# Performance work log

Measured on AMD Instinct MI355X. Metric: run time of the kernel, lower is better.

The kernel has to match this reference:

```python
import jax, jax.numpy as jnp
import numpy as np


def setup_inputs() -> dict:
    key = jax.random.key(0)
    k1, k2 = jax.random.split(key)
    B, T, D, K = 8, 4096, 256, 1024
    z = jax.random.normal(k1, (B, T, D), dtype=jnp.float32)
    codebook = jax.random.uniform(k2, (K, D), dtype=jnp.float32)
    return {"z": z, "codebook": codebook}


def reference(z, codebook):
    # Squared L2 distance via dot-product decomposition (same argmin as
    # the broadcasted squared-difference in the original module, without
    # materializing the (B,T,K,D) intermediate).
    #   ||z - c||^2 = ||z||^2 - 2 z.c + ||c||^2
    z_sq = jnp.sum(z * z, axis=-1, keepdims=True)            # (B,T,1)
    c_sq = jnp.sum(codebook * codebook, axis=-1)             # (K,)
    cross = jnp.einsum("btd,kd->btk", z, codebook)           # (B,T,K)
    l2_distance = z_sq - 2.0 * cross + c_sq                  # (B,T,K)
    codebook_indices = jnp.argmin(l2_distance, axis=-1)      # (B,T)
    z_q = codebook[codebook_indices]                         # (B,T,D)
    # Straight-through estimator
    z_q = z + jax.lax.stop_gradient(z_q - z)
    return (z_q, codebook_indices)
```

## Files before the change

### kernel.cpp

```cpp
#include <hip/hip_runtime.h>
#include <math.h>

#define NTOK   32768
#define NDIM   256
#define NCODE  1024
#define NSTRIP 8
#define CHUNK  (128 * 32)

typedef _Float16 f16x8 __attribute__((ext_vector_type(8)));
typedef float    f32x4 __attribute__((ext_vector_type(4)));

__device__ __forceinline__ void gld_lds16(const void* g, void* l) {
    __builtin_amdgcn_global_load_lds(
        (const __attribute__((address_space(1))) void*)g,
        (__attribute__((address_space(3))) void*)l, 16, 0, 0);
}

__global__ __launch_bounds__(256) void prep_cb(
        const float* __restrict__ cb,
        _Float16* __restrict__ ch, _Float16* __restrict__ cl,
        float* __restrict__ csq) {
    const int L   = blockIdx.x * 256 + threadIdx.x;
    const int row = L >> 5;
    const int g   = L & 31;

    const float* src = cb + (size_t)row * NDIM + g * 8;
    float4 a0 = *(const float4*)src;
    float4 a1 = *(const float4*)(src + 4);
    float v[8] = {a0.x, a0.y, a0.z, a0.w, a1.x, a1.y, a1.z, a1.w};
    f16x8 hi, lo;
    float s = 0.f;
    #pragma unroll
    for (int e = 0; e < 8; ++e) {
        _Float16 h = (_Float16)v[e];
        hi[e] = h;
        lo[e] = (_Float16)(v[e] - (float)h);
        s += v[e] * v[e];
    }
    const size_t dst = (size_t)((row >> 7) * 8 + (g >> 2)) * CHUNK
                     + (row & 127) * 32 + (g & 3) * 8;
    *(f16x8*)&ch[dst] = hi;
    *(f16x8*)&cl[dst] = lo;
    #pragma unroll
    for (int off = 16; off > 0; off >>= 1) s += __shfl_down(s, off, 32);
    if ((threadIdx.x & 31) == 0) csq[row] = s;
}

__global__ __launch_bounds__(256, 2) void vq_main(
        const float* __restrict__ z,
        const _Float16* __restrict__ ch, const _Float16* __restrict__ cl,
        const float* __restrict__ csq, const float* __restrict__ cb,
        float* __restrict__ zq, float* __restrict__ io) {
    __shared__ _Float16 Bh[4 * CHUNK];
    __shared__ _Float16 Bl[4 * CHUNK];

    const int tid  = threadIdx.x;
    const int w    = tid >> 6;
    const int lane = tid & 63;
    const int quad = lane >> 4, lr = lane & 15;
    const int my   = w >> 1, nx = w & 1;
    const int m0   = blockIdx.x * 64;

    f16x8 ah[2][8], al[2][8];
    #pragma unroll
    for (int mt = 0; mt < 2; ++mt) {
        const float* zp = z + (size_t)(m0 + my * 32 + mt * 16 + lr) * NDIM
                        + quad * 8;
        #pragma unroll
        for (int c = 0; c < 8; ++c) {
            float4 a0 = *(const float4*)(zp + c * 32);
            float4 a1 = *(const float4*)(zp + c * 32 + 4);
            float v[8] = {a0.x, a0.y, a0.z, a0.w, a1.x, a1.y, a1.z, a1.w};
            #pragma unroll
            for (int e = 0; e < 8; ++e) {
                _Float16 h = (_Float16)v[e];
                ah[mt][c][e] = h;
                al[mt][c][e] = (_Float16)(v[e] - (float)h);
            }
        }
    }

    float bv[2][4];
    int   bi[2][4];
    #pragma unroll
    for (int mt = 0; mt < 2; ++mt)
        #pragma unroll
        for (int r = 0; r < 4; ++r) { bv[mt][r] = INFINITY; bi[mt][r] = 0x7fffffff; }

    f32x4 acc[2][4];
    #pragma unroll
    for (int mt = 0; mt < 2; ++mt)
        #pragma unroll
        for (int t = 0; t < 4; ++t) acc[mt][t] = (f32x4){0.f, 0.f, 0.f, 0.f};

    for (int strip = 0; strip < NSTRIP; ++strip) {
        float cs[4];
        #pragma unroll
        for (int t = 0; t < 4; ++t)
            cs[t] = csq[strip * 128 + (nx * 4 + t) * 16 + lr];

        #pragma unroll
        for (int kh = 0; kh < 2; ++kh) {
            __syncthreads();
            {
                const size_t base = (size_t)(strip * 8 + kh * 4 + w) * CHUNK
                                  + lane * 8;
                const _Float16* sh = ch + base;
                const _Float16* sl = cl + base;
                #pragma unroll
                for (int i = 0; i < 8; ++i) {
                    gld_lds16(sh + i * 512, Bh + w * CHUNK + i * 512);
                    gld_lds16(sl + i * 512, Bl + w * CHUNK + i * 512);
                }
            }
            __syncthreads();

            #pragma unroll
            for (int k4 = 0; k4 < 4; ++k4) {
                const int kg = kh * 4 + k4;
                f16x8 fbh[4], fbl[4];
                #pragma unroll
                for (int t = 0; t < 4; ++t) {
                    const int off = k4 * CHUNK
                                  + ((nx * 4 + t) * 16 + lr) * 32 + quad * 8;
                    fbh[t] = *(const f16x8*)&Bh[off];
                    fbl[t] = *(const f16x8*)&Bl[off];
                }
                #pragma unroll
                for (int mt = 0; mt < 2; ++mt)
                    #pragma unroll
                    for (int t = 0; t < 4; ++t) {
                        acc[mt][t] = __builtin_amdgcn_mfma_f32_16x16x32_f16(
                                         ah[mt][kg], fbh[t], acc[mt][t], 0, 0, 0);
                        acc[mt][t] = __builtin_amdgcn_mfma_f32_16x16x32_f16(
                                         al[mt][kg], fbh[t], acc[mt][t], 0, 0, 0);
                        acc[mt][t] = __builtin_amdgcn_mfma_f32_16x16x32_f16(
                                         ah[mt][kg], fbl[t], acc[mt][t], 0, 0, 0);
                    }
            }
        }

        #pragma unroll
        for (int mt = 0; mt < 2; ++mt)
            #pragma unroll
            for (int r = 0; r < 4; ++r)
                #pragma unroll
                for (int t = 0; t < 4; ++t) {
                    float v = cs[t] - 2.0f * acc[mt][t][r];
                    int   n = strip * 128 + (nx * 4 + t) * 16 + lr;
                    if (v < bv[mt][r] || (v == bv[mt][r] && n < bi[mt][r])) {
                        bv[mt][r] = v; bi[mt][r] = n;
                    }
                }
        #pragma unroll
        for (int mt = 0; mt < 2; ++mt)
            #pragma unroll
            for (int t = 0; t < 4; ++t) acc[mt][t] = (f32x4){0.f, 0.f, 0.f, 0.f};
    }

    #pragma unroll
    for (int msk = 1; msk < 16; msk <<= 1)
        #pragma unroll
        for (int mt = 0; mt < 2; ++mt)
            #pragma unroll
            for (int r = 0; r < 4; ++r) {
                float ov = __shfl_xor(bv[mt][r], msk, 64);
                int   oi = __shfl_xor(bi[mt][r], msk, 64);
                if (ov < bv[mt][r] || (ov == bv[mt][r] && oi < bi[mt][r])) {
                    bv[mt][r] = ov; bi[mt][r] = oi;
                }
            }

    __syncthreads();
    float* sval  = (float*)Bh;
    int*   sidx  = (int*)&Bh[512];
    int*   bestS = (int*)&Bh[1024];

    if (lr == 0) {
        #pragma unroll
        for (int mt = 0; mt < 2; ++mt)
            #pragma unroll
            for (int r = 0; r < 4; ++r) {
                int row = my * 32 + mt * 16 + quad * 4 + r;
                sval[row * 2 + nx] = bv[mt][r];
                sidx[row * 2 + nx] = bi[mt][r];
            }
    }
    __syncthreads();

    if (tid < 64) {
        float v0 = sval[tid * 2], v1 = sval[tid * 2 + 1];
        int   i0 = sidx[tid * 2], i1 = sidx[tid * 2 + 1];
        bool take1 = (v1 < v0) || (v1 == v0 && i1 < i0);
        int best = take1 ? i1 : i0;
        bestS[tid] = best;
        io[m0 + tid] = (float)best;
    }
    __syncthreads();

    const int tr = tid >> 4, tc = tid & 15;
    #pragma unroll
    for (int p = 0; p < 4; ++p) {
        int row = p * 16 + tr;
        const float* src = cb + (size_t)bestS[row] * NDIM;
        float*       dst = zq + (size_t)(m0 + row) * NDIM;
        #pragma unroll
        for (int q = 0; q < 4; ++q) {
            int col = q * 64 + tc * 4;
            *(float4*)&dst[col] = *(const float4*)&src[col];
        }
    }
}

extern "C" void kernel_launch(void* const* d_in, const int* in_sizes, int n_in,
                              void* d_out, int out_size, void* d_ws, size_t ws_size,
                              hipStream_t stream) {
    const float* z  = (const float*)d_in[0];
    const float* cb = (const float*)d_in[1];

    float* zq = (float*)d_out;
    float* io = (float*)d_out + (size_t)NTOK * NDIM;

    _Float16* ch  = (_Float16*)d_ws;
    _Float16* cl  = ch + (size_t)NCODE * NDIM;
    float*    csq = (float*)(cl + (size_t)NCODE * NDIM);

    prep_cb<<<NCODE * 32 / 256, 256, 0, stream>>>(cb, ch, cl, csq);

    vq_main<<<NTOK / 64, 256, 0, stream>>>(z, ch, cl, csq, cb, zq, io);
}
```

Measured before the change: 132.6 us.

## Double-buffer codebook LDS tiles with 512-thread blocks and conflict-free layout

Blocks grow to 512 threads covering 128 tokens, so each codebook tile staged in LDS is reused by twice as many rows. The codebook hi/lo tiles are now double-buffered: the next half-strip is issued with global_load_lds while the current one is consumed, using explicit vmcnt waits and raw barriers in place of a full sync pair. The packed codebook layout is rearranged so each lane's 16-byte LDS reads are contiguous, which is meant to cut bank conflicts, and MFMA bursts raise wave priority with s_setprio. LDS use doubles to 128 KB per block, which with launch_bounds(512,2) may limit occupancy, and the hand-set vmcnt counts depend on the exact number of loads issued.

```diff
diff --git a/kernel.cpp b/kernel.cpp
--- a/kernel.cpp
+++ b/kernel.cpp
@@ -4,8 +4,7 @@
 #define NTOK   32768
 #define NDIM   256
 #define NCODE  1024
-#define NSTRIP 8
-#define CHUNK  (128 * 32)
+#define CHUNK  4096
 
 typedef _Float16 f16x8 __attribute__((ext_vector_type(8)));
 typedef float    f32x4 __attribute__((ext_vector_type(4)));
@@ -37,8 +36,9 @@
         lo[e] = (_Float16)(v[e] - (float)h);
         s += v[e] * v[e];
     }
+    const int r = row & 127;
     const size_t dst = (size_t)((row >> 7) * 8 + (g >> 2)) * CHUNK
-                     + (row & 127) * 32 + (g & 3) * 8;
+                     + (r >> 4) * 512 + (g & 3) * 128 + (r & 15) * 8;
     *(f16x8*)&ch[dst] = hi;
     *(f16x8*)&cl[dst] = lo;
     #pragma unroll
@@ -46,20 +46,60 @@
     if ((threadIdx.x & 31) == 0) csq[row] = s;
 }
 
-__global__ __launch_bounds__(256, 2) void vq_main(
+
+#define STAGE(h, buf)                                                          \
+    do {                                                                       \
+        const size_t _sb = (size_t)(h) * 16384 + (size_t)tid * 8;              \
+        _Pragma("unroll")                                                      \
+        for (int _i = 0; _i < 4; ++_i) {                                       \
+            gld_lds16(ch + _sb + _i * 4096, &Bs[buf][0][w * 512 + _i * 4096]); \
+            gld_lds16(cl + _sb + _i * 4096, &Bs[buf][1][w * 512 + _i * 4096]); \
+        }                                                                      \
+    } while (0)
+
+#define COMPUTE(kh, buf)                                                       \
+    do {                                                                       \
+        _Pragma("unroll")                                                      \
+        for (int _k4 = 0; _k4 < 4; ++_k4) {                                    \
+            f16x8 fbh[4], fbl[4];                                              \
+            _Pragma("unroll")                                                  \
+            for (int _t = 0; _t < 4; ++_t) {                                   \
+                const int _off = _k4 * 4096 + (nx * 4 + _t) * 512              \
+                               + quad * 128 + lr * 8;                          \
+                fbh[_t] = *(const f16x8*)&Bs[buf][0][_off];                    \
+                fbl[_t] = *(const f16x8*)&Bs[buf][1][_off];                    \
+            }                                                                  \
+            __builtin_amdgcn_s_setprio(1);                                     \
+            _Pragma("unroll")                                                  \
+            for (int _mt = 0; _mt < 2; ++_mt)                                  \
+                _Pragma("unroll")                                              \
+                for (int _t = 0; _t < 4; ++_t) {                               \
+                    acc[_mt][_t] = __builtin_amdgcn_mfma_f32_16x16x32_f16(     \
+                        ah[_mt][(kh) * 4 + _k4], fbh[_t], acc[_mt][_t], 0, 0, 0); \
+                    acc[_mt][_t] = __builtin_amdgcn_mfma_f32_16x16x32_f16(     \
+                        al[_mt][(kh) * 4 + _k4], fbh[_t], acc[_mt][_t], 0, 0, 0); \
+                    acc[_mt][_t] = __builtin_amdgcn_mfma_f32_16x16x32_f16(     \
+                        ah[_mt][(kh) * 4 + _k4], fbl[_t], acc[_mt][_t], 0, 0, 0); \
+                }                                                              \
+            __builtin_amdgcn_s_setprio(0);                                     \
+        }                                                                      \
+    } while (0)
+
+__global__ __launch_bounds__(512, 2) void vq_main(
         const float* __restrict__ z,
         const _Float16* __restrict__ ch, const _Float16* __restrict__ cl,
         const float* __restrict__ csq, const float* __restrict__ cb,
         float* __restrict__ zq, float* __restrict__ io) {
-    __shared__ _Float16 Bh[4 * CHUNK];
-    __shared__ _Float16 Bl[4 * CHUNK];
+    __shared__ _Float16 Bs[2][2][16384];
 
     const int tid  = threadIdx.x;
     const int w    = tid >> 6;
     const int lane = tid & 63;
     const int quad = lane >> 4, lr = lane & 15;
     const int my   = w >> 1, nx = w & 1;
-    const int m0   = blockIdx.x * 64;
+    const int m0   = blockIdx.x * 128;
+
+    STAGE(0, 0);
 
     f16x8 ah[2][8], al[2][8];
     #pragma unroll
@@ -93,52 +133,31 @@
         #pragma unroll
         for (int t = 0; t < 4; ++t) acc[mt][t] = (f32x4){0.f, 0.f, 0.f, 0.f};
 
-    for (int strip = 0; strip < NSTRIP; ++strip) {
+    for (int strip = 0; strip < 8; ++strip) {
         float cs[4];
         #pragma unroll
         for (int t = 0; t < 4; ++t)
             cs[t] = csq[strip * 128 + (nx * 4 + t) * 16 + lr];
 
-        #pragma unroll
-        for (int kh = 0; kh < 2; ++kh) {
-            __syncthreads();
-            {
-                const size_t base = (size_t)(strip * 8 + kh * 4 + w) * CHUNK
-                                  + lane * 8;
-                const _Float16* sh = ch + base;
-                const _Float16* sl = cl + base;
-                #pragma unroll
-                for (int i = 0; i < 8; ++i) {
-                    gld_lds16(sh + i * 512, Bh + w * CHUNK + i * 512);
-                    gld_lds16(sl + i * 512, Bl + w * CHUNK + i * 512);
-                }
-            }
-            __syncthreads();
-
-            #pragma unroll
-            for (int k4 = 0; k4 < 4; ++k4) {
-                const int kg = kh * 4 + k4;
-                f16x8 fbh[4], fbl[4];
-                #pragma unroll
-                for (int t = 0; t < 4; ++t) {
-                    const int off = k4 * CHUNK
-                                  + ((nx * 4 + t) * 16 + lr) * 32 + quad * 8;
-                    fbh[t] = *(const f16x8*)&Bh[off];
-                    fbl[t] = *(const f16x8*)&Bl[off];
-                }
-                #pragma unroll
-                for (int mt = 0; mt < 2; ++mt)
-                    #pragma unroll
-                    for (int t = 0; t < 4; ++t) {
-                        acc[mt][t] = __builtin_amdgcn_mfma_f32_16x16x32_f16(
-                                         ah[mt][kg], fbh[t], acc[mt][t], 0, 0, 0);
-                        acc[mt][t] = __builtin_amdgcn_mfma_f32_16x16x32_f16(
-                                         al[mt][kg], fbh[t], acc[mt][t], 0, 0, 0);
-                        acc[mt][t] = __builtin_amdgcn_mfma_f32_16x16x32_f16(
-                                         ah[mt][kg], fbl[t], acc[mt][t], 0, 0, 0);
-                    }
-            }
+        STAGE(2 * strip + 1, 1);
+        asm volatile("s_waitcnt vmcnt(12)" ::: "memory");
+        __builtin_amdgcn_s_barrier();
+        __builtin_amdgcn_sched_barrier(0);
+        COMPUTE(0, 0);
+        __builtin_amdgcn_sched_barrier(0);
+        __builtin_amdgcn_s_barrier();
+
+        if (strip < 7) {
+            STAGE(2 * strip + 2, 0);
+            asm volatile("s_waitcnt vmcnt(8)" ::: "memory");
+        } else {
+            asm volatile("s_waitcnt vmcnt(0)" ::: "memory");
         }
+        __builtin_amdgcn_s_barrier();
+        __builtin_amdgcn_sched_barrier(0);
+        COMPUTE(1, 1);
+        __builtin_amdgcn_sched_barrier(0);
+        __builtin_amdgcn_s_barrier();
 
         #pragma unroll
         for (int mt = 0; mt < 2; ++mt)
@@ -172,9 +191,9 @@
             }
 
     __syncthreads();
-    float* sval  = (float*)Bh;
-    int*   sidx  = (int*)&Bh[512];
-    int*   bestS = (int*)&Bh[1024];
+    float* sval  = (float*)&Bs[0][0][0];
+    int*   sidx  = (int*)(sval + 256);
+    int*   bestS = (int*)(sval + 512);
 
     if (lr == 0) {
         #pragma unroll
@@ -188,7 +207,7 @@
     }
     __syncthreads();
 
-    if (tid < 64) {
+    if (tid < 128) {
         float v0 = sval[tid * 2], v1 = sval[tid * 2 + 1];
         int   i0 = sidx[tid * 2], i1 = sidx[tid * 2 + 1];
         bool take1 = (v1 < v0) || (v1 == v0 && i1 < i0);
@@ -201,7 +220,7 @@
     const int tr = tid >> 4, tc = tid & 15;
     #pragma unroll
     for (int p = 0; p < 4; ++p) {
-        int row = p * 16 + tr;
+        int row = p * 32 + tr;
         const float* src = cb + (size_t)bestS[row] * NDIM;
         float*       dst = zq + (size_t)(m0 + row) * NDIM;
         #pragma unroll
@@ -227,5 +246,5 @@
 
     prep_cb<<<NCODE * 32 / 256, 256, 0, stream>>>(cb, ch, cl, csq);
 
-    vq_main<<<NTOK / 64, 256, 0, stream>>>(z, ch, cl, csq, cb, zq, io);
-}
+    vq_main<<<NTOK / 128, 512, 0, stream>>>(z, ch, cl, csq, cb, zq, io);
+}
```

Result: slower. 151.6 us (+14.3%).

## Pipeline codebook chunks through a 4-slot LDS ring with async prefetch

Applied to the files above, without the earlier changes.

Replaces the load-all-then-compute scheme (two syncthreads per 4-chunk batch) with a 4-deep ring buffer of per-k chunks. Each phase prefetches chunk p+3 with global_load_lds while computing on chunk p, using vmcnt waits and raw barriers. The codebook layout is reshuffled so each lane reads its fragment more contiguously, csq is staged in LDS, and MFMA blocks run at raised priority. The aim is to hide global-load latency behind MFMA work, at the cost of more barriers and tighter hand-managed wait counts.

```diff
diff --git a/kernel.cpp b/kernel.cpp
--- a/kernel.cpp
+++ b/kernel.cpp
@@ -4,8 +4,7 @@
 #define NTOK   32768
 #define NDIM   256
 #define NCODE  1024
-#define NSTRIP 8
-#define CHUNK  (128 * 32)
+#define CHUNK  4096
 
 typedef _Float16 f16x8 __attribute__((ext_vector_type(8)));
 typedef float    f32x4 __attribute__((ext_vector_type(4)));
@@ -37,22 +36,81 @@
         lo[e] = (_Float16)(v[e] - (float)h);
         s += v[e] * v[e];
     }
+    const int r = row & 127;
     const size_t dst = (size_t)((row >> 7) * 8 + (g >> 2)) * CHUNK
-                     + (row & 127) * 32 + (g & 3) * 8;
+                     + (r >> 4) * 512 + (g & 3) * 128 + (r & 15) * 8;
     *(f16x8*)&ch[dst] = hi;
     *(f16x8*)&cl[dst] = lo;
     #pragma unroll
     for (int off = 16; off > 0; off >>= 1) s += __shfl_down(s, off, 32);
     if ((threadIdx.x & 31) == 0) csq[row] = s;
 }
+
+
+#define PHASE(p, GB, DOSTAGE, WK, FIRSTZ) do {                               \
+    const int _sl = (p) & 3;                                                 \
+    f16x8 fbh[4], fbl[4];                                                    \
+    _Pragma("unroll")                                                        \
+    for (int _t = 0; _t < 4; ++_t) {                                         \
+        fbh[_t] = *(const f16x8*)&Bs[_sl][0][boff[_t]];                      \
+        fbl[_t] = *(const f16x8*)&Bs[_sl][1][boff[_t]];                      \
+    }                                                                        \
+    if (DOSTAGE) {                                                           \
+        const size_t _s  = (size_t)((GB) + (p) + 3) * CHUNK + tid * 8;       \
+        const int    _dsl = ((p) + 3) & 3;                                   \
+        const int    _d   = tid * 8;                                         \
+        gld_lds16(ch + _s,        &Bs[_dsl][0][_d]);                         \
+        gld_lds16(ch + _s + 2048, &Bs[_dsl][0][_d + 2048]);                  \
+        gld_lds16(cl + _s,        &Bs[_dsl][1][_d]);                         \
+        gld_lds16(cl + _s + 2048, &Bs[_dsl][1][_d + 2048]);                  \
+    }                                                                        \
+    asm volatile("s_waitcnt vmcnt(" #WK ")" ::: "memory");                   \
+    __builtin_amdgcn_s_barrier();                                            \
+    asm volatile("s_waitcnt lgkmcnt(0)" ::: "memory");                       \
+    __builtin_amdgcn_s_setprio(1);                                           \
+    _Pragma("unroll")                                                        \
+    for (int _mt = 0; _mt < 2; ++_mt)                                        \
+        _Pragma("unroll")                                                    \
+        for (int _t = 0; _t < 4; ++_t) {                                     \
+            acc[_mt][_t] = __builtin_amdgcn_mfma_f32_16x16x32_f16(           \
+                ah[_mt][(p)], fbh[_t],                                       \
+                (FIRSTZ) ? zz : acc[_mt][_t], 0, 0, 0);                      \
+            acc[_mt][_t] = __builtin_amdgcn_mfma_f32_16x16x32_f16(           \
+                al[_mt][(p)], fbh[_t], acc[_mt][_t], 0, 0, 0);               \
+            acc[_mt][_t] = __builtin_amdgcn_mfma_f32_16x16x32_f16(           \
+                ah[_mt][(p)], fbl[_t], acc[_mt][_t], 0, 0, 0);               \
+        }                                                                    \
+    __builtin_amdgcn_s_setprio(0);                                           \
+    __builtin_amdgcn_s_barrier();                                            \
+} while (0)
+
+#define FOLD(S) do {                                                         \
+    float cs[4];                                                             \
+    _Pragma("unroll")                                                        \
+    for (int _t = 0; _t < 4; ++_t)                                           \
+        cs[_t] = csq_lds[(S) * 128 + (nx * 4 + _t) * 16 + lr];               \
+    _Pragma("unroll")                                                        \
+    for (int _mt = 0; _mt < 2; ++_mt)                                        \
+        _Pragma("unroll")                                                    \
+        for (int _r = 0; _r < 4; ++_r)                                       \
+            _Pragma("unroll")                                                \
+            for (int _t = 0; _t < 4; ++_t) {                                 \
+                float _v = cs[_t] - 2.0f * acc[_mt][_t][_r];                 \
+                int   _n = (S) * 128 + (nx * 4 + _t) * 16 + lr;              \
+                if (_v < bv[_mt][_r] ||                                      \
+                    (_v == bv[_mt][_r] && _n < bi[_mt][_r])) {               \
+                    bv[_mt][_r] = _v; bi[_mt][_r] = _n;                      \
+                }                                                            \
+            }                                                                \
+} while (0)
 
 __global__ __launch_bounds__(256, 2) void vq_main(
         const float* __restrict__ z,
         const _Float16* __restrict__ ch, const _Float16* __restrict__ cl,
         const float* __restrict__ csq, const float* __restrict__ cb,
         float* __restrict__ zq, float* __restrict__ io) {
-    __shared__ _Float16 Bh[4 * CHUNK];
-    __shared__ _Float16 Bl[4 * CHUNK];
+    __shared__ _Float16 Bs[4][2][4096];
+    __shared__ float    csq_lds[1024];
 
     const int tid  = threadIdx.x;
     const int w    = tid >> 6;
@@ -60,6 +118,16 @@
     const int quad = lane >> 4, lr = lane & 15;
     const int my   = w >> 1, nx = w & 1;
     const int m0   = blockIdx.x * 64;
+
+    gld_lds16(csq + tid * 4, &csq_lds[tid * 4]);
+    #pragma unroll
+    for (int c = 0; c < 3; ++c) {
+        const size_t sb = (size_t)c * CHUNK + tid * 8;
+        gld_lds16(ch + sb,        &Bs[c][0][tid * 8]);
+        gld_lds16(ch + sb + 2048, &Bs[c][0][tid * 8 + 2048]);
+        gld_lds16(cl + sb,        &Bs[c][1][tid * 8]);
+        gld_lds16(cl + sb + 2048, &Bs[c][1][tid * 8 + 2048]);
+    }
 
     f16x8 ah[2][8], al[2][8];
     #pragma unroll
@@ -80,6 +148,11 @@
         }
     }
 
+    int boff[4];
+    #pragma unroll
+    for (int t = 0; t < 4; ++t)
+        boff[t] = (nx * 4 + t) * 512 + quad * 128 + lr * 8;
+
     float bv[2][4];
     int   bi[2][4];
     #pragma unroll
@@ -87,75 +160,39 @@
         #pragma unroll
         for (int r = 0; r < 4; ++r) { bv[mt][r] = INFINITY; bi[mt][r] = 0x7fffffff; }
 
+    const f32x4 zz = (f32x4){0.f, 0.f, 0.f, 0.f};
     f32x4 acc[2][4];
     #pragma unroll
     for (int mt = 0; mt < 2; ++mt)
         #pragma unroll
-        for (int t = 0; t < 4; ++t) acc[mt][t] = (f32x4){0.f, 0.f, 0.f, 0.f};
-
-    for (int strip = 0; strip < NSTRIP; ++strip) {
-        float cs[4];
-        #pragma unroll
-        for (int t = 0; t < 4; ++t)
-            cs[t] = csq[strip * 128 + (nx * 4 + t) * 16 + lr];
-
-        #pragma unroll
-        for (int kh = 0; kh < 2; ++kh) {
-            __syncthreads();
-            {
-                const size_t base = (size_t)(strip * 8 + kh * 4 + w) * CHUNK
-                                  + lane * 8;
-                const _Float16* sh = ch + base;
-                const _Float16* sl = cl + base;
-                #pragma unroll
-                for (int i = 0; i < 8; ++i) {
-                    gld_lds16(sh + i * 512, Bh + w * CHUNK + i * 512);
-                    gld_lds16(sl + i * 512, Bl + w * CHUNK + i * 512);
-                }
-            }
-            __syncthreads();
-
-            #pragma unroll
-            for (int k4 = 0; k4 < 4; ++k4) {
-                const int kg = kh * 4 + k4;
-                f16x8 fbh[4], fbl[4];
-                #pragma unroll
-                for (int t = 0; t < 4; ++t) {
-                    const int off = k4 * CHUNK
-                                  + ((nx * 4 + t) * 16 + lr) * 32 + quad * 8;
-                    fbh[t] = *(const f16x8*)&Bh[off];
-                    fbl[t] = *(const f16x8*)&Bl[off];
-                }
-                #pragma unroll
-                for (int mt = 0; mt < 2; ++mt)
-                    #pragma unroll
-                    for (int t = 0; t < 4; ++t) {
-                        acc[mt][t] = __builtin_amdgcn_mfma_f32_16x16x32_f16(
-                                         ah[mt][kg], fbh[t], acc[mt][t], 0, 0, 0);
-                        acc[mt][t] = __builtin_amdgcn_mfma_f32_16x16x32_f16(
-                                         al[mt][kg], fbh[t], acc[mt][t], 0, 0, 0);
-                        acc[mt][t] = __builtin_amdgcn_mfma_f32_16x16x32_f16(
-                                         ah[mt][kg], fbl[t], acc[mt][t], 0, 0, 0);
-                    }
-            }
-        }
-
-        #pragma unroll
-        for (int mt = 0; mt < 2; ++mt)
-            #pragma unroll
-            for (int r = 0; r < 4; ++r)
-                #pragma unroll
-                for (int t = 0; t < 4; ++t) {
-                    float v = cs[t] - 2.0f * acc[mt][t][r];
-                    int   n = strip * 128 + (nx * 4 + t) * 16 + lr;
-                    if (v < bv[mt][r] || (v == bv[mt][r] && n < bi[mt][r])) {
-                        bv[mt][r] = v; bi[mt][r] = n;
-                    }
-                }
-        #pragma unroll
-        for (int mt = 0; mt < 2; ++mt)
-            #pragma unroll
-            for (int t = 0; t < 4; ++t) acc[mt][t] = (f32x4){0.f, 0.f, 0.f, 0.f};
+        for (int t = 0; t < 4; ++t) acc[mt][t] = zz;
+
+    asm volatile("s_waitcnt vmcnt(0)" ::: "memory");
+    __syncthreads();
+
+    for (int s = 0; s < 7; ++s) {
+        const int gb = s * 8;
+        PHASE(0, gb, 1, 8, 1);
+        PHASE(1, gb, 1, 8, 0);
+        PHASE(2, gb, 1, 8, 0);
+        PHASE(3, gb, 1, 8, 0);
+        PHASE(4, gb, 1, 8, 0);
+        PHASE(5, gb, 1, 8, 0);
+        PHASE(6, gb, 1, 8, 0);
+        PHASE(7, gb, 1, 8, 0);
+        FOLD(s);
+    }
+    {
+        const int gb = 56;
+        PHASE(0, gb, 1, 8, 1);
+        PHASE(1, gb, 1, 8, 0);
+        PHASE(2, gb, 1, 8, 0);
+        PHASE(3, gb, 1, 8, 0);
+        PHASE(4, gb, 1, 8, 0);
+        PHASE(5, gb, 0, 4, 0);
+        PHASE(6, gb, 0, 0, 0);
+        PHASE(7, gb, 0, 0, 0);
+        FOLD(7);
     }
 
     #pragma unroll
@@ -172,9 +209,9 @@
             }
 
     __syncthreads();
-    float* sval  = (float*)Bh;
-    int*   sidx  = (int*)&Bh[512];
-    int*   bestS = (int*)&Bh[1024];
+    float* sval  = (float*)&Bs[0][0][0];
+    int*   sidx  = (int*)&Bs[0][0][512];
+    int*   bestS = (int*)&Bs[0][0][1024];
 
     if (lr == 0) {
         #pragma unroll
```

Measured after the change: 133.9 us. No clear change (+0.9%).

## Split-K across 16 waves with direct global fragment loads and LDS partial reduction

Applied to the files above, without the earlier changes.

Grows the block to 1024 threads and splits the 256-wide reduction dimension across two wave groups. Each wave loads codebook fragments straight from global memory in a pre-swizzled MFMA layout instead of staging them through LDS, and partial sums are combined through a double-buffered LDS exchange. It also raises MFMA issue priority around the compute. The aim is more waves to hide latency and the removal of the LDS staging traffic. In exchange it adds a barrier per strip, redundant global and L2 reads of the codebook, and a larger register footprint per thread under launch_bounds 1024.

```diff
diff --git a/kernel.cpp b/kernel.cpp
--- a/kernel.cpp
+++ b/kernel.cpp
@@ -4,17 +4,10 @@
 #define NTOK   32768
 #define NDIM   256
 #define NCODE  1024
-#define NSTRIP 8
-#define CHUNK  (128 * 32)
+#define CHUNK  4096
 
 typedef _Float16 f16x8 __attribute__((ext_vector_type(8)));
 typedef float    f32x4 __attribute__((ext_vector_type(4)));
-
-__device__ __forceinline__ void gld_lds16(const void* g, void* l) {
-    __builtin_amdgcn_global_load_lds(
-        (const __attribute__((address_space(1))) void*)g,
-        (__attribute__((address_space(3))) void*)l, 16, 0, 0);
-}
 
 __global__ __launch_bounds__(256) void prep_cb(
         const float* __restrict__ cb,
@@ -37,8 +30,9 @@
         lo[e] = (_Float16)(v[e] - (float)h);
         s += v[e] * v[e];
     }
+    const int r = row & 127;
     const size_t dst = (size_t)((row >> 7) * 8 + (g >> 2)) * CHUNK
-                     + (row & 127) * 32 + (g & 3) * 8;
+                     + (r >> 4) * 512 + (g & 3) * 128 + (r & 15) * 8;
     *(f16x8*)&ch[dst] = hi;
     *(f16x8*)&cl[dst] = lo;
     #pragma unroll
@@ -46,28 +40,30 @@
     if ((threadIdx.x & 31) == 0) csq[row] = s;
 }
 
-__global__ __launch_bounds__(256, 2) void vq_main(
+__global__ __launch_bounds__(1024) void vq_main(
         const float* __restrict__ z,
         const _Float16* __restrict__ ch, const _Float16* __restrict__ cl,
         const float* __restrict__ csq, const float* __restrict__ cb,
         float* __restrict__ zq, float* __restrict__ io) {
-    __shared__ _Float16 Bh[4 * CHUNK];
-    __shared__ _Float16 Bl[4 * CHUNK];
+    __shared__ float mbuf[2][8][64][16];
 
     const int tid  = threadIdx.x;
     const int w    = tid >> 6;
     const int lane = tid & 63;
     const int quad = lane >> 4, lr = lane & 15;
-    const int my   = w >> 1, nx = w & 1;
+    const int kh   = w >> 3;
+    const int my   = (w >> 2) & 1;
+    const int nx   = w & 3;
+    const int w4   = (my << 2) | nx;
     const int m0   = blockIdx.x * 64;
 
-    f16x8 ah[2][8], al[2][8];
+    f16x8 ah[2][4], al[2][4];
     #pragma unroll
     for (int mt = 0; mt < 2; ++mt) {
         const float* zp = z + (size_t)(m0 + my * 32 + mt * 16 + lr) * NDIM
-                        + quad * 8;
-        #pragma unroll
-        for (int c = 0; c < 8; ++c) {
+                        + kh * 128 + quad * 8;
+        #pragma unroll
+        for (int c = 0; c < 4; ++c) {
             float4 a0 = *(const float4*)(zp + c * 32);
             float4 a1 = *(const float4*)(zp + c * 32 + 4);
             float v[8] = {a0.x, a0.y, a0.z, a0.w, a1.x, a1.y, a1.z, a1.w};
@@ -80,6 +76,9 @@
         }
     }
 
+    const int boff0 = (nx * 2) * 512 + quad * 128 + lr * 8;
+    const int boff1 = boff0 + 512;
+
     float bv[2][4];
     int   bi[2][4];
     #pragma unroll
@@ -87,128 +86,128 @@
         #pragma unroll
         for (int r = 0; r < 4; ++r) { bv[mt][r] = INFINITY; bi[mt][r] = 0x7fffffff; }
 
-    f32x4 acc[2][4];
-    #pragma unroll
-    for (int mt = 0; mt < 2; ++mt)
-        #pragma unroll
-        for (int t = 0; t < 4; ++t) acc[mt][t] = (f32x4){0.f, 0.f, 0.f, 0.f};
-
-    for (int strip = 0; strip < NSTRIP; ++strip) {
-        float cs[4];
-        #pragma unroll
-        for (int t = 0; t < 4; ++t)
-            cs[t] = csq[strip * 128 + (nx * 4 + t) * 16 + lr];
-
-        #pragma unroll
-        for (int kh = 0; kh < 2; ++kh) {
-            __syncthreads();
-            {
-                const size_t base = (size_t)(strip * 8 + kh * 4 + w) * CHUNK
-                                  + lane * 8;
-                const _Float16* sh = ch + base;
-                const _Float16* sl = cl + base;
+    const f32x4 zz = (f32x4){0.f, 0.f, 0.f, 0.f};
+    f32x4 acc[2][2];
+
+    for (int s = 0; s < 8; ++s) {
+        const size_t cbase = (size_t)(s * 8 + kh * 4) * CHUNK;
+        #pragma unroll
+        for (int c = 0; c < 4; ++c) {
+            const _Float16* ph = ch + cbase + (size_t)c * CHUNK;
+            const _Float16* pl = cl + cbase + (size_t)c * CHUNK;
+            f16x8 bh0 = *(const f16x8*)&ph[boff0];
+            f16x8 bh1 = *(const f16x8*)&ph[boff1];
+            f16x8 bl0 = *(const f16x8*)&pl[boff0];
+            f16x8 bl1 = *(const f16x8*)&pl[boff1];
+            __builtin_amdgcn_s_setprio(1);
+            #pragma unroll
+            for (int mt = 0; mt < 2; ++mt) {
+                acc[mt][0] = __builtin_amdgcn_mfma_f32_16x16x32_f16(
+                    ah[mt][c], bh0, (c == 0) ? zz : acc[mt][0], 0, 0, 0);
+                acc[mt][0] = __builtin_amdgcn_mfma_f32_16x16x32_f16(
+                    al[mt][c], bh0, acc[mt][0], 0, 0, 0);
+                acc[mt][0] = __builtin_amdgcn_mfma_f32_16x16x32_f16(
+                    ah[mt][c], bl0, acc[mt][0], 0, 0, 0);
+                acc[mt][1] = __builtin_amdgcn_mfma_f32_16x16x32_f16(
+                    ah[mt][c], bh1, (c == 0) ? zz : acc[mt][1], 0, 0, 0);
+                acc[mt][1] = __builtin_amdgcn_mfma_f32_16x16x32_f16(
+                    al[mt][c], bh1, acc[mt][1], 0, 0, 0);
+                acc[mt][1] = __builtin_amdgcn_mfma_f32_16x16x32_f16(
+                    ah[mt][c], bl1, acc[mt][1], 0, 0, 0);
+            }
+            __builtin_amdgcn_s_setprio(0);
+        }
+
+        const int par = s & 1;
+        if (kh) {
+            float* mp = &mbuf[par][w4][lane][0];
+            *(f32x4*)(mp +  0) = acc[0][0];
+            *(f32x4*)(mp +  4) = acc[0][1];
+            *(f32x4*)(mp +  8) = acc[1][0];
+            *(f32x4*)(mp + 12) = acc[1][1];
+        }
+        __syncthreads();
+        if (!kh) {
+            float cs0 = csq[s * 128 + (nx * 2) * 16 + lr];
+            float cs1 = csq[s * 128 + (nx * 2 + 1) * 16 + lr];
+            const float* mp = &mbuf[par][w4][lane][0];
+            f32x4 p00 = *(const f32x4*)(mp +  0);
+            f32x4 p01 = *(const f32x4*)(mp +  4);
+            f32x4 p10 = *(const f32x4*)(mp +  8);
+            f32x4 p11 = *(const f32x4*)(mp + 12);
+            #pragma unroll
+            for (int mt = 0; mt < 2; ++mt) {
+                f32x4 d0 = (mt == 0) ? p00 : p10;
+                f32x4 d1 = (mt == 0) ? p01 : p11;
                 #pragma unroll
-                for (int i = 0; i < 8; ++i) {
-                    gld_lds16(sh + i * 512, Bh + w * CHUNK + i * 512);
-                    gld_lds16(sl + i * 512, Bl + w * CHUNK + i * 512);
-                }
-            }
-            __syncthreads();
-
-            #pragma unroll
-            for (int k4 = 0; k4 < 4; ++k4) {
-                const int kg = kh * 4 + k4;
-                f16x8 fbh[4], fbl[4];
-                #pragma unroll
-                for (int t = 0; t < 4; ++t) {
-                    const int off = k4 * CHUNK
-                                  + ((nx * 4 + t) * 16 + lr) * 32 + quad * 8;
-                    fbh[t] = *(const f16x8*)&Bh[off];
-                    fbl[t] = *(const f16x8*)&Bl[off];
-                }
-                #pragma unroll
-                for (int mt = 0; mt < 2; ++mt)
-                    #pragma unroll
-                    for (int t = 0; t < 4; ++t) {
-                        acc[mt][t] = __builtin_amdgcn_mfma_f32_16x16x32_f16(
-                                         ah[mt][kg], fbh[t], acc[mt][t], 0, 0, 0);
-                        acc[mt][t] = __builtin_amdgcn_mfma_f32_16x16x32_f16(
-                                         al[mt][kg], fbh[t], acc[mt][t], 0, 0, 0);
-                        acc[mt][t] = __builtin_amdgcn_mfma_f32_16x16x32_f16(
-                                         ah[mt][kg], fbl[t], acc[mt][t], 0, 0, 0);
+                for (int r = 0; r < 4; ++r) {
+                    float v0 = cs0 - 2.0f * (acc[mt][0][r] + d0[r]);
+                    int   n0 = s * 128 + (nx * 2) * 16 + lr;
+                    if (v0 < bv[mt][r] || (v0 == bv[mt][r] && n0 < bi[mt][r])) {
+                        bv[mt][r] = v0; bi[mt][r] = n0;
                     }
-            }
-        }
-
-        #pragma unroll
-        for (int mt = 0; mt < 2; ++mt)
-            #pragma unroll
-            for (int r = 0; r < 4; ++r)
-                #pragma unroll
-                for (int t = 0; t < 4; ++t) {
-                    float v = cs[t] - 2.0f * acc[mt][t][r];
-                    int   n = strip * 128 + (nx * 4 + t) * 16 + lr;
-                    if (v < bv[mt][r] || (v == bv[mt][r] && n < bi[mt][r])) {
-                        bv[mt][r] = v; bi[mt][r] = n;
+                    float v1 = cs1 - 2.0f * (acc[mt][1][r] + d1[r]);
+                    int   n1 = s * 128 + (nx * 2 + 1) * 16 + lr;
+                    if (v1 < bv[mt][r] || (v1 == bv[mt][r] && n1 < bi[mt][r])) {
+                        bv[mt][r] = v1; bi[mt][r] = n1;
                     }
                 }
-        #pragma unroll
-        for (int mt = 0; mt < 2; ++mt)
-            #pragma unroll
-            for (int t = 0; t < 4; ++t) acc[mt][t] = (f32x4){0.f, 0.f, 0.f, 0.f};
-    }
-
-    #pragma unroll
-    for (int msk = 1; msk < 16; msk <<= 1)
-        #pragma unroll
-        for (int mt = 0; mt < 2; ++mt)
-            #pragma unroll
-            for (int r = 0; r < 4; ++r) {
-                float ov = __shfl_xor(bv[mt][r], msk, 64);
-                int   oi = __shfl_xor(bi[mt][r], msk, 64);
-                if (ov < bv[mt][r] || (ov == bv[mt][r] && oi < bi[mt][r])) {
-                    bv[mt][r] = ov; bi[mt][r] = oi;
+            }
+        }
+    }
+
+    if (!kh) {
+        #pragma unroll
+        for (int msk = 1; msk < 16; msk <<= 1)
+            #pragma unroll
+            for (int mt = 0; mt < 2; ++mt)
+                #pragma unroll
+                for (int r = 0; r < 4; ++r) {
+                    float ov = __shfl_xor(bv[mt][r], msk, 64);
+                    int   oi = __shfl_xor(bi[mt][r], msk, 64);
+                    if (ov < bv[mt][r] || (ov == bv[mt][r] && oi < bi[mt][r])) {
+                        bv[mt][r] = ov; bi[mt][r] = oi;
+                    }
                 }
-            }
-
-    __syncthreads();
-    float* sval  = (float*)Bh;
-    int*   sidx  = (int*)&Bh[512];
-    int*   bestS = (int*)&Bh[1024];
-
-    if (lr == 0) {
+    }
+
+    float* sval  = &mbuf[0][0][0][0];
+    int*   sidx  = (int*)(sval + 256);
+    int*   bestS = (int*)(sval + 512);
+
+    if (!kh && lr == 0) {
         #pragma unroll
         for (int mt = 0; mt < 2; ++mt)
             #pragma unroll
             for (int r = 0; r < 4; ++r) {
                 int row = my * 32 + mt * 16 + quad * 4 + r;
-                sval[row * 2 + nx] = bv[mt][r];
-                sidx[row * 2 + nx] = bi[mt][r];
+                sval[row * 4 + nx] = bv[mt][r];
+                sidx[row * 4 + nx] = bi[mt][r];
             }
     }
     __syncthreads();
 
     if (tid < 64) {
-        float v0 = sval[tid * 2], v1 = sval[tid * 2 + 1];
-        int   i0 = sidx[tid * 2], i1 = sidx[tid * 2 + 1];
-        bool take1 = (v1 < v0) || (v1 == v0 && i1 < i0);
-        int best = take1 ? i1 : i0;
-        bestS[tid] = best;
-        io[m0 + tid] = (float)best;
+        float bvv = sval[tid * 4];
+        int   bii = sidx[tid * 4];
+        #pragma unroll
+        for (int k = 1; k < 4; ++k) {
+            float v = sval[tid * 4 + k];
+            int   i = sidx[tid * 4 + k];
+            if (v < bvv || (v == bvv && i < bii)) { bvv = v; bii = i; }
+        }
+        bestS[tid] = bii;
+        io[m0 + tid] = (float)bii;
     }
     __syncthreads();
 
     const int tr = tid >> 4, tc = tid & 15;
-    #pragma unroll
-    for (int p = 0; p < 4; ++p) {
-        int row = p * 16 + tr;
-        const float* src = cb + (size_t)bestS[row] * NDIM;
-        float*       dst = zq + (size_t)(m0 + row) * NDIM;
-        #pragma unroll
-        for (int q = 0; q < 4; ++q) {
-            int col = q * 64 + tc * 4;
-            *(float4*)&dst[col] = *(const float4*)&src[col];
-        }
+    const float* src = cb + (size_t)bestS[tr] * NDIM;
+    float*       dst = zq + (size_t)(m0 + tr) * NDIM;
+    #pragma unroll
+    for (int q = 0; q < 4; ++q) {
+        int col = q * 64 + tc * 4;
+        *(float4*)&dst[col] = *(const float4*)&src[col];
     }
 }
 
@@ -227,5 +226,5 @@
 
     prep_cb<<<NCODE * 32 / 256, 256, 0, stream>>>(cb, ch, cl, csq);
 
-    vq_main<<<NTOK / 64, 256, 0, stream>>>(z, ch, cl, csq, cb, zq, io);
+    vq_main<<<NTOK / 64, 1024, 0, stream>>>(z, ch, cl, csq, cb, zq, io);
 }
```

Result: slower. 188.2 us (+41.9%).
